# Kernel optimization log

Measured on AMD Instinct MI355X. Metric: run time of the kernel, lower is better.

## Reference

```python
import jax, jax.numpy as jnp
import numpy as np

K = 1024       # num_embeddings
D = 64         # embedding_dim
DECAY = 0.99
COMMIT = 0.25
EPS = 1e-05


def setup_inputs() -> dict:
    key = jax.random.key(0)
    k1, k2, k3 = jax.random.split(key, 3)
    x = jax.random.normal(k1, (16, 64, 64, 64), jnp.float32)  # NCHW, C == D
    embedding_weight = jax.random.normal(k2, (K, D), jnp.float32)
    ema_weight = jax.random.normal(k3, (K, D), jnp.float32)
    ema_cluster_size = jnp.zeros((K,), jnp.float32)
    return {"x": x, "embedding_weight": embedding_weight,
            "ema_cluster_size": ema_cluster_size, "ema_weight": ema_weight}


def reference(x, embedding_weight, ema_cluster_size, ema_weight):
    # NCHW -> NHWC, flatten tokens
    xp = jnp.transpose(x, (0, 2, 3, 1))            # [B,H,W,D]
    flat = xp.reshape(-1, D)                        # [N,D]
    dists = ((flat ** 2).sum(1, keepdims=True)
             + (embedding_weight ** 2).sum(1)
             - 2.0 * flat @ embedding_weight.T)     # [N,K]
    idx = jnp.argmin(dists, axis=1)                 # [N]
    encodings = jax.nn.one_hot(idx, K, dtype=flat.dtype)  # [N,K]
    quantized = jnp.take(embedding_weight, idx, axis=0).reshape(xp.shape)
    # training-mode EMA updates (scatter-add instead of dense one-hot matmuls)
    counts = jnp.zeros((K,), flat.dtype).at[idx].add(1.0)
    new_cs = ema_cluster_size * DECAY + (1.0 - DECAY) * counts
    n = new_cs.sum()
    new_cs = (new_cs + EPS) / (n + K * EPS) * n     # Laplace smoothing
    dw = jnp.zeros((K, D), flat.dtype).at[idx].add(flat)
    new_ema_weight = ema_weight * DECAY + (1.0 - DECAY) * dw
    new_embedding = new_ema_weight / new_cs[:, None]
    # commitment loss and straight-through estimator
    e_latent_loss = jnp.mean((jax.lax.stop_gradient(quantized) - xp) ** 2)
    loss = COMMIT * e_latent_loss
    q_st = xp + jax.lax.stop_gradient(quantized - xp)
    return (loss, jnp.transpose(q_st, (0, 3, 1, 2)), encodings,
            new_embedding, new_cs, new_ema_weight)
```

## Files before the change

### kernel.cpp

```cpp
#include <hip/hip_runtime.h>

#define DECAYF 0.99f
#define ONEMF 0.01f
#define EPSF 1e-5f

typedef __bf16 bf16x8 __attribute__((ext_vector_type(8)));
typedef float f32x4 __attribute__((ext_vector_type(4)));
typedef unsigned short ushort8 __attribute__((ext_vector_type(8)));

#define WS_COUNTS 65536
#define WS_NCHALF 66560
#define WS_SSE    67584
#define WS_EHI    67600
#define WS_ELO    100368
#define WS_IDX    133136

__device__ __forceinline__ float wave_reduce_add(float v) {
#pragma unroll
    for (int o = 32; o > 0; o >>= 1) v += __shfl_xor(v, o, 64);
    return v;
}

__device__ __forceinline__ unsigned short bf_rne(float f) {
    unsigned int u = __float_as_uint(f);
    unsigned int r = u + 0x7fffu + ((u >> 16) & 1u);
    return (unsigned short)(r >> 16);
}

__global__ __launch_bounds__(256) void prep_kernel(const float* __restrict__ E,
                                                   float* __restrict__ ws) {
    const int bid = blockIdx.x, tid = threadIdx.x;
    const int id = bid * 256 + tid;
    ws[id] = 0.0f;
    if (bid < 4) ws[WS_COUNTS + bid * 256 + tid] = 0.0f;
    if (bid == 4 && tid == 0) ws[WS_SSE] = 0.0f;
    const float v = E[id];
    const unsigned short h = bf_rne(v);
    const float hf = __uint_as_float((unsigned int)h << 16);
    const unsigned short l = bf_rne(v - hf);
    ((unsigned short*)(ws + WS_EHI))[id] = h;
    ((unsigned short*)(ws + WS_ELO))[id] = l;
    const int lane = tid & 63;
    const float s = wave_reduce_add(v * v);
    if (lane == 0) ws[WS_NCHALF + (id >> 6)] = -0.5f * s;
}

__global__ __launch_bounds__(256) void vq_score(const float* __restrict__ x,
                                                const float* __restrict__ E,
                                                float* __restrict__ ws) {
    const int tid = threadIdx.x;
    const int lane = tid & 63;
    const int w = tid >> 6;
    const int blk = blockIdx.x;
    const int b = blk >> 5;
    const int hw0 = (blk & 31) << 7;
    const int tok0 = blk << 7;

    __shared__ float xs[128 * 68];
    __shared__ int i1sh[128], i2sh[128];

    {
        const float* xb = x + ((size_t)b << 18) + hw0;
#pragma unroll
        for (int cc = 0; cc < 32; ++cc) {
            const int id = cc * 256 + tid;
            const int c = id >> 7, t = id & 127;
            xs[t * 68 + c] = xb[((size_t)c << 12) + t];
        }
    }
    __syncthreads();

    const int q = lane >> 4, m = lane & 15;

    bf16x8 Ah[2][2], Al[2][2];
#pragma unroll
    for (int t = 0; t < 2; ++t) {
        const int tok = w * 32 + t * 16 + m;
#pragma unroll
        for (int s = 0; s < 2; ++s) {
            const float* p = &xs[tok * 68 + s * 32 + q * 8];
            ushort8 hu, lu;
#pragma unroll
            for (int j = 0; j < 8; ++j) {
                const float f = p[j];
                const unsigned short h = bf_rne(f);
                const float hf = __uint_as_float((unsigned int)h << 16);
                hu[j] = h;
                lu[j] = bf_rne(f - hf);
            }
            Ah[t][s] = __builtin_bit_cast(bf16x8, hu);
            Al[t][s] = __builtin_bit_cast(bf16x8, lu);
        }
    }

    const ushort8* __restrict__ Ehp = (const ushort8*)(ws + WS_EHI);
    const ushort8* __restrict__ Elp = (const ushort8*)(ws + WS_ELO);
    const float* __restrict__ ncp = ws + WS_NCHALF;

    float b1[2][4], b2[2][4];
    int i1[2][4], i2[2][4];
#pragma unroll
    for (int t = 0; t < 2; ++t)
#pragma unroll
        for (int r = 0; r < 4; ++r) { b1[t][r] = -1e30f; b2[t][r] = -1e30f; i1[t][r] = 0; i2[t][r] = 1; }

    ushort8 p0h[2], p1h[2], p0l[2], p1l[2];
    float pnc[2];
#pragma unroll
    for (int s = 0; s < 2; ++s) {
        const int code = s * 16 + m;
        p0h[s] = Ehp[code * 8 + q];
        p1h[s] = Ehp[code * 8 + 4 + q];
        p0l[s] = Elp[code * 8 + q];
        p1l[s] = Elp[code * 8 + 4 + q];
        pnc[s] = ncp[code];
    }

#define VQ_STEP(S, CK)                                                          \
    {                                                                           \
        const bf16x8 bh0 = __builtin_bit_cast(bf16x8, p0h[S]);                  \
        const bf16x8 bh1 = __builtin_bit_cast(bf16x8, p1h[S]);                  \
        const bf16x8 bl0 = __builtin_bit_cast(bf16x8, p0l[S]);                  \
        const bf16x8 bl1 = __builtin_bit_cast(bf16x8, p1l[S]);                  \
        const float nc = pnc[S];                                                \
        if ((CK) + 2 < 64) {                                                    \
            const int code = ((CK) + 2) * 16 + m;                               \
            p0h[S] = Ehp[code * 8 + q];                                         \
            p1h[S] = Ehp[code * 8 + 4 + q];                                     \
            p0l[S] = Elp[code * 8 + q];                                         \
            p1l[S] = Elp[code * 8 + 4 + q];                                     \
            pnc[S] = ncp[code];                                                 \
        }                                                                       \
        const int idx = (CK) * 16 + m;                                          \
        _Pragma("unroll")                                                       \
        for (int t = 0; t < 2; ++t) {                                           \
            f32x4 acc = {nc, nc, nc, nc};         \
            acc = __builtin_amdgcn_mfma_f32_16x16x32_bf16(Ah[t][0], bh0, acc, 0, 0, 0); \
            acc = __builtin_amdgcn_mfma_f32_16x16x32_bf16(Ah[t][1], bh1, acc, 0, 0, 0); \
            acc = __builtin_amdgcn_mfma_f32_16x16x32_bf16(Al[t][0], bh0, acc, 0, 0, 0); \
            acc = __builtin_amdgcn_mfma_f32_16x16x32_bf16(Al[t][1], bh1, acc, 0, 0, 0); \
            acc = __builtin_amdgcn_mfma_f32_16x16x32_bf16(Ah[t][0], bl0, acc, 0, 0, 0); \
            acc = __builtin_amdgcn_mfma_f32_16x16x32_bf16(Ah[t][1], bl1, acc, 0, 0, 0); \
            _Pragma("unroll")                                                   \
            for (int r = 0; r < 4; ++r) {                                       \
                const float s = acc[r];                                         \
                const bool cA = s > b1[t][r];                                   \
                const bool cB = s > b2[t][r];                                   \
                b2[t][r] = cA ? b1[t][r] : (cB ? s : b2[t][r]);                 \
                i2[t][r] = cA ? i1[t][r] : (cB ? idx : i2[t][r]);               \
                b1[t][r] = cA ? s : b1[t][r];                                   \
                i1[t][r] = cA ? idx : i1[t][r];                                 \
            }                                                                   \
        }                                                                       \
    }

    for (int j = 0; j < 32; ++j) {
        VQ_STEP(0, 2 * j)
        VQ_STEP(1, 2 * j + 1)
    }
#undef VQ_STEP

#pragma unroll
    for (int d = 1; d < 16; d <<= 1) {
#pragma unroll
        for (int t = 0; t < 2; ++t)
#pragma unroll
            for (int r = 0; r < 4; ++r) {
                const float ob1 = __shfl_xor(b1[t][r], d, 64);
                const int   oi1 = __shfl_xor(i1[t][r], d, 64);
                const float ob2 = __shfl_xor(b2[t][r], d, 64);
                const int   oi2 = __shfl_xor(i2[t][r], d, 64);
                const bool wv = ob1 > b1[t][r];
                const float t1 = wv ? ob1 : b1[t][r]; const int ti1 = wv ? oi1 : i1[t][r];
                const float sA = wv ? b1[t][r] : ob1; const int siA = wv ? i1[t][r] : oi1;
                const float sB = wv ? ob2 : b2[t][r]; const int siB = wv ? oi2 : i2[t][r];
                const bool w2 = sB > sA;
                b1[t][r] = t1; i1[t][r] = ti1;
                b2[t][r] = w2 ? sB : sA; i2[t][r] = w2 ? siB : siA;
            }
    }
    if (m == 0) {
#pragma unroll
        for (int t = 0; t < 2; ++t)
#pragma unroll
            for (int r = 0; r < 4; ++r) {
                const int tokL = w * 32 + t * 16 + q * 4 + r;
                i1sh[tokL] = i1[t][r];
                i2sh[tokL] = i2[t][r];
            }
    }

    float dval = 0.0f;
    if (lane < 32) {
        const int tokL = w * 32 + lane;
        const int I1 = i1sh[tokL], I2 = i2sh[tokL];
        const int ca = I1 < I2 ? I1 : I2;
        const int cb = I1 < I2 ? I2 : I1;
        const float* Ea = E + ca * 64;
        const float* Eb = E + cb * 64;
        const float* xr = &xs[tokL * 68];
        double sa = 0, ea = 0, sb = 0, eb = 0, x2 = 0;
#pragma unroll 8
        for (int c = 0; c < 64; ++c) {
            const double xv = (double)xr[c];
            const double va = (double)Ea[c], vb = (double)Eb[c];
            sa += xv * va; ea += va * va;
            sb += xv * vb; eb += vb * vb;
            x2 += xv * xv;
        }
        const double qa = ea - 2.0 * sa;
        const double qb = eb - 2.0 * sb;
        int best; double qq;
        if (qb < qa) { best = cb; qq = qb; } else { best = ca; qq = qa; }
        ((int*)(ws + WS_IDX))[tok0 + tokL] = best;
        float dd = (float)(qq + x2);
        dval = dd < 0.f ? 0.f : dd;
        atomicAdd(&ws[WS_COUNTS + best], 1.0f);
    }
    const float ssum = wave_reduce_add(dval);
    if (lane == 0) atomicAdd(&ws[WS_SSE], ssum);
}

__global__ __launch_bounds__(256) void vq_out(const float* __restrict__ x,
                                              const float* __restrict__ E,
                                              float* __restrict__ out,
                                              float* __restrict__ ws) {
    const int tid = threadIdx.x;
    const int lane = tid & 63;
    const int w = tid >> 6;
    const int blk = blockIdx.x;
    const int b = blk >> 7;
    const int hw0 = (blk & 127) << 5;
    const int tok0 = blk << 5;

    __shared__ float xsb[32 * 65];
    __shared__ float eqb[32 * 65];
    __shared__ int idxb[32];

    if (tid < 32) idxb[tid] = ((const int*)(ws + WS_IDX))[tok0 + tid];
    {
        const float* xb = x + ((size_t)b << 18) + hw0;
#pragma unroll
        for (int cc = 0; cc < 8; ++cc) {
            const int id = cc * 256 + tid;
            const int t = id & 31, c = id >> 5;
            xsb[t * 65 + c] = xb[((size_t)c << 12) + t];
        }
    }
    __syncthreads();
#pragma unroll
    for (int j = 0; j < 8; ++j) {
        const int t = w * 8 + j;
        eqb[t * 65 + lane] = E[idxb[t] * 64 + lane];
    }
    __syncthreads();

    float* outq = out + 1;
#pragma unroll
    for (int cc = 0; cc < 8; ++cc) {
        const int c = cc * 8 + (tid >> 5);
        const int t = tid & 31;
        const float xv = xsb[t * 65 + c];
        const float eq = eqb[t * 65 + c];
        outq[((size_t)(b * 64 + c) << 12) + hw0 + t] = xv + (eq - xv);
    }

    {
        float* enc = out + 1 + (size_t)4194304;
        const int c0 = tid << 2;
        for (int t = 0; t < 32; ++t) {
            const int kb = idxb[t];
            f32x4 v;
            v[0] = (c0 == kb) ? 1.0f : 0.0f;
            v[1] = (c0 + 1 == kb) ? 1.0f : 0.0f;
            v[2] = (c0 + 2 == kb) ? 1.0f : 0.0f;
            v[3] = (c0 + 3 == kb) ? 1.0f : 0.0f;
            __builtin_nontemporal_store(v, (f32x4*)(enc + (size_t)(tok0 + t) * 1024 + c0));
        }
    }

#pragma unroll
    for (int j = 0; j < 8; ++j) {
        const int t = w * 8 + j;
        const int kb = idxb[t];
        atomicAdd(&ws[kb * 64 + lane], xsb[t * 65 + lane]);
    }
}

__global__ __launch_bounds__(1024) void fin_cs(const float* __restrict__ cs_in,
                                               float* __restrict__ out,
                                               const float* __restrict__ ws) {
    __shared__ float red[16];
    __shared__ float n_sh;
    const int tid = threadIdx.x;
    const float raw = cs_in[tid] * DECAYF + ONEMF * ws[WS_COUNTS + tid];
    const float s = wave_reduce_add(raw);
    if ((tid & 63) == 0) red[tid >> 6] = s;
    __syncthreads();
    if (tid == 0) {
        float n = 0.f;
#pragma unroll
        for (int i = 0; i < 16; ++i) n += red[i];
        n_sh = n;
        out[0] = 0.25f * ws[WS_SSE] * (1.0f / 4194304.0f);
    }
    __syncthreads();
    const float n = n_sh;
    out[71368705 + tid] = (raw + EPSF) / (n + 1024.0f * EPSF) * n;
}

__global__ __launch_bounds__(256) void fin_w(const float* __restrict__ emaw,
                                             float* __restrict__ out,
                                             const float* __restrict__ ws) {
    const int i = blockIdx.x * 256 + threadIdx.x;
    const float val = emaw[i] * DECAYF + ONEMF * ws[i];
    out[71369729 + i] = val;
    const float cs = out[71368705 + (i >> 6)];
    out[71303169 + i] = val / cs;
}

extern "C" void kernel_launch(void* const* d_in, const int* in_sizes, int n_in,
                              void* d_out, int out_size, void* d_ws, size_t ws_size,
                              hipStream_t stream) {
    const float* x    = (const float*)d_in[0];
    const float* E    = (const float*)d_in[1];
    const float* cs   = (const float*)d_in[2];
    const float* emaw = (const float*)d_in[3];
    float* out = (float*)d_out;
    float* ws  = (float*)d_ws;

    prep_kernel<<<256, 256, 0, stream>>>(E, ws);
    vq_score<<<512, 256, 0, stream>>>(x, E, ws);
    vq_out<<<2048, 256, 0, stream>>>(x, E, out, ws);
    fin_cs<<<1, 1024, 0, stream>>>(cs, out, ws);
    fin_w<<<256, 256, 0, stream>>>(emaw, out, ws);
}
```

Baseline: 422.1 us.

## Replace scatter-add atomics with ballot-based per-code gather reduction kernel

Per-code sums and counts are no longer built with global atomicAdd scatter. vq_out now writes a token-major copy of x into the workspace, and a new vq_dw kernel assigns four codes per block. Each wave scans the index array, uses ballots to find matching tokens, sums their rows and reduces across waves. This removes contention on hot codebook rows but adds an extra 16 MB write and gathered read, plus a full scan of all indices by every block. The old atomic path stays as a fallback when the workspace is too small.

```diff
diff --git a/kernel.cpp b/kernel.cpp
--- a/kernel.cpp
+++ b/kernel.cpp
@@ -14,6 +14,8 @@
 #define WS_EHI    67600
 #define WS_ELO    100368
 #define WS_IDX    133136
+#define WS_XT     198672
+#define WS_NEED_BYTES ((size_t)(WS_XT + 4194304) * 4)
 
 __device__ __forceinline__ float wave_reduce_add(float v) {
 #pragma unroll
@@ -215,16 +217,15 @@
         ((int*)(ws + WS_IDX))[tok0 + tokL] = best;
         float dd = (float)(qq + x2);
         dval = dd < 0.f ? 0.f : dd;
-        atomicAdd(&ws[WS_COUNTS + best], 1.0f);
     }
     const float ssum = wave_reduce_add(dval);
     if (lane == 0) atomicAdd(&ws[WS_SSE], ssum);
 }
 
-__global__ __launch_bounds__(256) void vq_out(const float* __restrict__ x,
-                                              const float* __restrict__ E,
-                                              float* __restrict__ out,
-                                              float* __restrict__ ws) {
+__global__ __launch_bounds__(256) void vq_out_clean(const float* __restrict__ x,
+                                                    const float* __restrict__ E,
+                                                    float* __restrict__ out,
+                                                    float* __restrict__ ws) {
     const int tid = threadIdx.x;
     const int lane = tid & 63;
     const int w = tid >> 6;
@@ -252,6 +253,15 @@
     for (int j = 0; j < 8; ++j) {
         const int t = w * 8 + j;
         eqb[t * 65 + lane] = E[idxb[t] * 64 + lane];
+    }
+    {
+        float* xt = ws + WS_XT;
+#pragma unroll
+        for (int cc = 0; cc < 8; ++cc) {
+            const int id = cc * 256 + tid;
+            const int t = id >> 6, c = id & 63;
+            xt[(size_t)(tok0 + t) * 64 + c] = xsb[t * 65 + c];
+        }
     }
     __syncthreads();
 
@@ -278,12 +288,122 @@
             __builtin_nontemporal_store(v, (f32x4*)(enc + (size_t)(tok0 + t) * 1024 + c0));
         }
     }
-
+}
+
+__global__ __launch_bounds__(1024) void vq_dw(float* __restrict__ ws) {
+    const int tid = threadIdx.x;
+    const int wv = tid >> 6;
+    const int lane = tid & 63;
+    const int k0 = blockIdx.x * 4;
+    const int* __restrict__ idxp = (const int*)(ws + WS_IDX);
+    const float* __restrict__ xt = ws + WS_XT;
+
+    float a0 = 0.f, a1 = 0.f, a2 = 0.f, a3 = 0.f;
+    int c0 = 0, c1 = 0, c2 = 0, c3 = 0;
+    const int tbase = wv << 12;
+
+    for (int it = 0; it < 64; ++it) {
+        const int trow = tbase + (it << 6);
+        const int v = idxp[trow + lane];
+        unsigned long long m0 = __ballot(v == k0);
+        unsigned long long m1 = __ballot(v == k0 + 1);
+        unsigned long long m2 = __ballot(v == k0 + 2);
+        unsigned long long m3 = __ballot(v == k0 + 3);
+        c0 += __popcll(m0); c1 += __popcll(m1);
+        c2 += __popcll(m2); c3 += __popcll(m3);
+        while (m0) { const int bít = __builtin_ctzll(m0); m0 &= m0 - 1;
+                     a0 += xt[(size_t)(trow + bít) * 64 + lane]; }
+        while (m1) { const int bít = __builtin_ctzll(m1); m1 &= m1 - 1;
+                     a1 += xt[(size_t)(trow + bít) * 64 + lane]; }
+        while (m2) { const int bít = __builtin_ctzll(m2); m2 &= m2 - 1;
+                     a2 += xt[(size_t)(trow + bít) * 64 + lane]; }
+        while (m3) { const int bít = __builtin_ctzll(m3); m3 &= m3 - 1;
+                     a3 += xt[(size_t)(trow + bít) * 64 + lane]; }
+    }
+
+    __shared__ float red[16][4][64];
+    __shared__ int redc[16][4];
+    red[wv][0][lane] = a0; red[wv][1][lane] = a1;
+    red[wv][2][lane] = a2; red[wv][3][lane] = a3;
+    if (lane == 0) { redc[wv][0] = c0; redc[wv][1] = c1; redc[wv][2] = c2; redc[wv][3] = c3; }
+    __syncthreads();
+    if (tid < 256) {
+        const int c = tid >> 6, l = tid & 63;
+        float s = 0.f;
+#pragma unroll
+        for (int i = 0; i < 16; ++i) s += red[i][c][l];
+        ws[(k0 + c) * 64 + l] = s;
+    }
+    if (tid < 4) {
+        int s = 0;
+#pragma unroll
+        for (int i = 0; i < 16; ++i) s += redc[i][tid];
+        ws[WS_COUNTS + k0 + tid] = (float)s;
+    }
+}
+
+__global__ __launch_bounds__(256) void vq_out_atomic(const float* __restrict__ x,
+                                                     const float* __restrict__ E,
+                                                     float* __restrict__ out,
+                                                     float* __restrict__ ws) {
+    const int tid = threadIdx.x;
+    const int lane = tid & 63;
+    const int w = tid >> 6;
+    const int blk = blockIdx.x;
+    const int b = blk >> 7;
+    const int hw0 = (blk & 127) << 5;
+    const int tok0 = blk << 5;
+
+    __shared__ float xsb[32 * 65];
+    __shared__ float eqb[32 * 65];
+    __shared__ int idxb[32];
+
+    if (tid < 32) idxb[tid] = ((const int*)(ws + WS_IDX))[tok0 + tid];
+    {
+        const float* xb = x + ((size_t)b << 18) + hw0;
+#pragma unroll
+        for (int cc = 0; cc < 8; ++cc) {
+            const int id = cc * 256 + tid;
+            const int t = id & 31, c = id >> 5;
+            xsb[t * 65 + c] = xb[((size_t)c << 12) + t];
+        }
+    }
+    __syncthreads();
+#pragma unroll
+    for (int j = 0; j < 8; ++j) {
+        const int t = w * 8 + j;
+        eqb[t * 65 + lane] = E[idxb[t] * 64 + lane];
+    }
+    __syncthreads();
+
+    float* outq = out + 1;
+#pragma unroll
+    for (int cc = 0; cc < 8; ++cc) {
+        const int c = cc * 8 + (tid >> 5);
+        const int t = tid & 31;
+        const float xv = xsb[t * 65 + c];
+        const float eq = eqb[t * 65 + c];
+        outq[((size_t)(b * 64 + c) << 12) + hw0 + t] = xv + (eq - xv);
+    }
+    {
+        float* enc = out + 1 + (size_t)4194304;
+        const int c0 = tid << 2;
+        for (int t = 0; t < 32; ++t) {
+            const int kb = idxb[t];
+            f32x4 v;
+            v[0] = (c0 == kb) ? 1.0f : 0.0f;
+            v[1] = (c0 + 1 == kb) ? 1.0f : 0.0f;
+            v[2] = (c0 + 2 == kb) ? 1.0f : 0.0f;
+            v[3] = (c0 + 3 == kb) ? 1.0f : 0.0f;
+            __builtin_nontemporal_store(v, (f32x4*)(enc + (size_t)(tok0 + t) * 1024 + c0));
+        }
+    }
 #pragma unroll
     for (int j = 0; j < 8; ++j) {
         const int t = w * 8 + j;
         const int kb = idxb[t];
         atomicAdd(&ws[kb * 64 + lane], xsb[t * 65 + lane]);
+        if (lane == 0) atomicAdd(&ws[WS_COUNTS + kb], 1.0f);
     }
 }
 
@@ -331,7 +451,12 @@
 
     prep_kernel<<<256, 256, 0, stream>>>(E, ws);
     vq_score<<<512, 256, 0, stream>>>(x, E, ws);
-    vq_out<<<2048, 256, 0, stream>>>(x, E, out, ws);
+    if (ws_size >= WS_NEED_BYTES) {
+        vq_out_clean<<<2048, 256, 0, stream>>>(x, E, out, ws);
+        vq_dw<<<256, 1024, 0, stream>>>(ws);
+    } else {
+        vq_out_atomic<<<2048, 256, 0, stream>>>(x, E, out, ws);
+    }
     fin_cs<<<1, 1024, 0, stream>>>(cs, out, ws);
     fin_w<<<256, 256, 0, stream>>>(emaw, out, ws);
 }
```

After: 471.9 us. +11.8%, slower.

## Fuse scoring and output kernels, interleave one-hot zeroing with MFMA loop

Applied to the files above, without the earlier changes.

Merges vq_score and vq_out into one kernel, so the argmin indices stay in shared memory and x is loaded once instead of twice. The zeros of the one-hot encodings are written inside the code-scan loop, overlapping that large store stream with MFMA compute; each token's 1.0 is scattered afterwards. This drops a kernel launch and the re-read of x and indices. In exchange only 512 blocks now carry the 256 MB encoding write, and the 1.0 store must land after the zero store to the same address.

```diff
diff --git a/kernel.cpp b/kernel.cpp
--- a/kernel.cpp
+++ b/kernel.cpp
@@ -13,7 +13,6 @@
 #define WS_SSE    67584
 #define WS_EHI    67600
 #define WS_ELO    100368
-#define WS_IDX    133136
 
 __device__ __forceinline__ float wave_reduce_add(float v) {
 #pragma unroll
@@ -45,9 +44,10 @@
     if (lane == 0) ws[WS_NCHALF + (id >> 6)] = -0.5f * s;
 }
 
-__global__ __launch_bounds__(256) void vq_score(const float* __restrict__ x,
-                                                const float* __restrict__ E,
-                                                float* __restrict__ ws) {
+__global__ __launch_bounds__(256, 2) void vq_main(const float* __restrict__ x,
+                                                  const float* __restrict__ E,
+                                                  float* __restrict__ out,
+                                                  float* __restrict__ ws) {
     const int tid = threadIdx.x;
     const int lane = tid & 63;
     const int w = tid >> 6;
@@ -57,7 +57,10 @@
     const int tok0 = blk << 7;
 
     __shared__ float xs[128 * 68];
-    __shared__ int i1sh[128], i2sh[128];
+    __shared__ int i1sh[128], i2sh[128], idx_sh[128];
+
+    float* enc = out + 1 + (size_t)4194304;
+    f32x4* encb4 = (f32x4*)(enc + (size_t)tok0 * 1024);
 
     {
         const float* xb = x + ((size_t)b << 18) + hw0;
@@ -115,6 +118,8 @@
         p1l[s] = Elp[code * 8 + 4 + q];
         pnc[s] = ncp[code];
     }
+
+    const f32x4 z4 = {0.0f, 0.0f, 0.0f, 0.0f};
 
 #define VQ_STEP(S, CK)                                                          \
     {                                                                           \
@@ -130,6 +135,12 @@
             p0l[S] = Elp[code * 8 + q];                                         \
             p1l[S] = Elp[code * 8 + 4 + q];                                     \
             pnc[S] = ncp[code];                                                 \
+        }                                                                       \
+           \
+        {                                                                       \
+            const int zslot = (CK) * 512 + tid;                                 \
+            __builtin_nontemporal_store(z4, encb4 + zslot);                     \
+            __builtin_nontemporal_store(z4, encb4 + zslot + 256);               \
         }                                                                       \
         const int idx = (CK) * 16 + m;                                          \
         _Pragma("unroll")                                                       \
@@ -212,78 +223,36 @@
         const double qb = eb - 2.0 * sb;
         int best; double qq;
         if (qb < qa) { best = cb; qq = qb; } else { best = ca; qq = qa; }
-        ((int*)(ws + WS_IDX))[tok0 + tokL] = best;
+        idx_sh[tokL] = best;
         float dd = (float)(qq + x2);
         dval = dd < 0.f ? 0.f : dd;
         atomicAdd(&ws[WS_COUNTS + best], 1.0f);
     }
     const float ssum = wave_reduce_add(dval);
     if (lane == 0) atomicAdd(&ws[WS_SSE], ssum);
-}
-
-__global__ __launch_bounds__(256) void vq_out(const float* __restrict__ x,
-                                              const float* __restrict__ E,
-                                              float* __restrict__ out,
-                                              float* __restrict__ ws) {
-    const int tid = threadIdx.x;
-    const int lane = tid & 63;
-    const int w = tid >> 6;
-    const int blk = blockIdx.x;
-    const int b = blk >> 7;
-    const int hw0 = (blk & 127) << 5;
-    const int tok0 = blk << 5;
-
-    __shared__ float xsb[32 * 65];
-    __shared__ float eqb[32 * 65];
-    __shared__ int idxb[32];
-
-    if (tid < 32) idxb[tid] = ((const int*)(ws + WS_IDX))[tok0 + tid];
+    __syncthreads();
+
+    float* outq = out + 1;
+#pragma unroll
+    for (int cc = 0; cc < 32; ++cc) {
+        const int id = cc * 256 + tid;
+        const int c = id >> 7, t = id & 127;
+        const int kb = idx_sh[t];
+        const float xv = xs[t * 68 + c];
+        const float eq = E[kb * 64 + c];
+        outq[((size_t)(b * 64 + c) << 12) + hw0 + t] = xv + (eq - xv);
+    }
+#pragma unroll 4
+    for (int tt = 0; tt < 32; ++tt) {
+        const int t = w * 32 + tt;
+        const int kb = idx_sh[t];
+        atomicAdd(&ws[kb * 64 + lane], xs[t * 68 + lane]);
+    }
     {
-        const float* xb = x + ((size_t)b << 18) + hw0;
-#pragma unroll
-        for (int cc = 0; cc < 8; ++cc) {
-            const int id = cc * 256 + tid;
-            const int t = id & 31, c = id >> 5;
-            xsb[t * 65 + c] = xb[((size_t)c << 12) + t];
+        if (tid < 128) {
+            const int kb = idx_sh[tid];
+            __builtin_nontemporal_store(1.0f, enc + (size_t)(tok0 + tid) * 1024 + kb);
         }
-    }
-    __syncthreads();
-#pragma unroll
-    for (int j = 0; j < 8; ++j) {
-        const int t = w * 8 + j;
-        eqb[t * 65 + lane] = E[idxb[t] * 64 + lane];
-    }
-    __syncthreads();
-
-    float* outq = out + 1;
-#pragma unroll
-    for (int cc = 0; cc < 8; ++cc) {
-        const int c = cc * 8 + (tid >> 5);
-        const int t = tid & 31;
-        const float xv = xsb[t * 65 + c];
-        const float eq = eqb[t * 65 + c];
-        outq[((size_t)(b * 64 + c) << 12) + hw0 + t] = xv + (eq - xv);
-    }
-
-    {
-        float* enc = out + 1 + (size_t)4194304;
-        const int c0 = tid << 2;
-        for (int t = 0; t < 32; ++t) {
-            const int kb = idxb[t];
-            f32x4 v;
-            v[0] = (c0 == kb) ? 1.0f : 0.0f;
-            v[1] = (c0 + 1 == kb) ? 1.0f : 0.0f;
-            v[2] = (c0 + 2 == kb) ? 1.0f : 0.0f;
-            v[3] = (c0 + 3 == kb) ? 1.0f : 0.0f;
-            __builtin_nontemporal_store(v, (f32x4*)(enc + (size_t)(tok0 + t) * 1024 + c0));
-        }
-    }
-
-#pragma unroll
-    for (int j = 0; j < 8; ++j) {
-        const int t = w * 8 + j;
-        const int kb = idxb[t];
-        atomicAdd(&ws[kb * 64 + lane], xsb[t * 65 + lane]);
     }
 }
 
@@ -330,8 +299,7 @@
     float* ws  = (float*)d_ws;
 
     prep_kernel<<<256, 256, 0, stream>>>(E, ws);
-    vq_score<<<512, 256, 0, stream>>>(x, E, ws);
-    vq_out<<<2048, 256, 0, stream>>>(x, E, out, ws);
+    vq_main<<<512, 256, 0, stream>>>(x, E, out, ws);
     fin_cs<<<1, 1024, 0, stream>>>(cs, out, ws);
     fin_w<<<256, 256, 0, stream>>>(emaw, out, ws);
 }
```

Result: faster. 381.4 us (-9.6%).
